# Optimization experiments

Hardware: AMD Instinct MI355X
Metric: run time of the kernel (lower is better)

## Reference

```python
import jax, jax.numpy as jnp
import numpy as np

# NF4 codebook (bitsandbytes nf4 data type, 16 levels)
NF4_TABLE = np.array([
    -1.0, -0.6961928009986877, -0.5250730514526367, -0.39491748809814453,
    -0.28444138169288635, -0.18477343022823334, -0.09105003625154495, 0.0,
    0.07958029955625534, 0.16093020141124725, 0.24611230194568634,
    0.33791524171829224, 0.44070982933044434, 0.5626170039176941,
    0.7229568362236023, 1.0], dtype=np.float32)

BLOCKSIZE = 64
SCALING = 32.0 / 16.0  # lora_alpha / r


def setup_inputs() -> dict:
    key = jax.random.key(0)
    k1, k2, k3, k4, k5 = jax.random.split(key, 5)
    tokens, in_f, out_f, r = 256, 4096, 11008, 16
    x = jax.random.normal(k1, (tokens, in_f), dtype=jnp.float32)
    q_codes = jax.random.randint(k2, (out_f, in_f), 0, 16, dtype=jnp.int32)
    absmax = jax.random.uniform(k3, (out_f, in_f // BLOCKSIZE), dtype=jnp.float32)
    lora_A = jax.random.normal(k4, (r, in_f), dtype=jnp.float32) * (1.0 / np.sqrt(in_f))
    lora_B = jax.random.normal(k5, (out_f, r), dtype=jnp.float32) * 0.02
    return {"x": x, "q_codes": q_codes, "absmax": absmax,
            "lora_A": lora_A, "lora_B": lora_B}


def reference(x, q_codes, absmax, lora_A, lora_B):
    out_f, in_f = q_codes.shape
    nf4 = jnp.asarray(NF4_TABLE, dtype=x.dtype)
    # Dequantize: codebook lookup, then per-block absmax scale.
    W = nf4[q_codes].reshape(out_f, in_f // BLOCKSIZE, BLOCKSIZE)
    W = (W * absmax[:, :, None]).reshape(out_f, in_f)  # [out_f, in_f]
    # Base 4-bit linear (no bias in bnb Linear4bit default here).
    base = x @ W.T  # [tokens, out_f]
    # LoRA path: dropout p=0 is identity in eval; scaling = alpha/r.
    lora = (x @ lora_A.T) @ lora_B.T  # [tokens, r] -> [tokens, out_f]
    return base + lora * jnp.asarray(SCALING, dtype=x.dtype)
```

## Files before the change

kernel.cpp:

```cpp
#include <hip/hip_runtime.h>
#include <hip/hip_fp16.h>

typedef unsigned int uint;
typedef unsigned short ushort;

typedef __attribute__((ext_vector_type(8))) _Float16 f16x8;
typedef __attribute__((ext_vector_type(4))) float f32x4;

#define TOK 256
#define OUTF 11008
#define INF 4096
#define BM 256
#define BN 64
#define NT2 172

__device__ __constant__ float NF4_TBL[16] = {
    -1.0f, -0.6961928009986877f, -0.5250730514526367f, -0.39491748809814453f,
    -0.28444138169288635f, -0.18477343022823334f, -0.09105003625154495f, 0.0f,
    0.07958029955625534f, 0.16093020141124725f, 0.24611230194568634f,
    0.33791524171829224f, 0.44070982933044434f, 0.5626170039176941f,
    0.7229568362236023f, 1.0f};

__device__ __forceinline__ ushort f2h(float f) {
  return __half_as_ushort(__float2half(f));
}

__device__ __forceinline__ void async_cp16(const void* g, void* l) {
  __builtin_amdgcn_global_load_lds(
      (const __attribute__((address_space(1))) uint*)g,
      (__attribute__((address_space(3))) uint*)l, 16, 0, 0);
}

__global__ void prep_kernel(const int4* __restrict__ qc4, uint* __restrict__ pk,
                            const float4* __restrict__ x4, ushort4* __restrict__ xh4,
                            const float4* __restrict__ lB4, ushort4* __restrict__ lBh4) {
  const int stride = gridDim.x * blockDim.x;
  const int t0 = blockIdx.x * blockDim.x + threadIdx.x;
  for (int d = t0; d < OUTF * INF / 8; d += stride) {
    int4 a = qc4[2 * d];
    int4 b = qc4[2 * d + 1];
    pk[d] = (uint)(a.x & 15) | ((uint)(a.y & 15) << 4) | ((uint)(a.z & 15) << 8) |
            ((uint)(a.w & 15) << 12) | ((uint)(b.x & 15) << 16) | ((uint)(b.y & 15) << 20) |
            ((uint)(b.z & 15) << 24) | ((uint)(b.w & 15) << 28);
  }
  for (int i = t0; i < TOK * INF / 4; i += stride) {
    float4 v = x4[i];
    ushort4 o;
    o.x = f2h(v.x); o.y = f2h(v.y); o.z = f2h(v.z); o.w = f2h(v.w);
    xh4[i] = o;
  }
  for (int i = t0; i < OUTF * 16; i += stride) {
    int n = i >> 4, jq = i & 15;
    ushort4 o = {0, 0, 0, 0};
    if (jq < 4) {
      float4 v = lB4[n * 4 + jq];
      o.x = f2h(v.x); o.y = f2h(v.y); o.z = f2h(v.z); o.w = f2h(v.w);
    }
    lBh4[i] = o;
  }
}

__global__ __launch_bounds__(1024)
void xa_kernel(const float* __restrict__ x, const float* __restrict__ lA,
               ushort* __restrict__ xa2) {
  const int m = blockIdx.x;
  const int t = threadIdx.x;
  const float4* x4 = (const float4*)(x + (size_t)m * INF);
  const float4* lA4 = (const float4*)lA;
  float4 xv = x4[t];
  float acc[16];
#pragma unroll
  for (int j = 0; j < 16; ++j) {
    float4 a = lA4[j * (INF / 4) + t];
    acc[j] = xv.x * a.x + xv.y * a.y + xv.z * a.z + xv.w * a.w;
  }
#pragma unroll
  for (int j = 0; j < 16; ++j)
#pragma unroll
    for (int s = 32; s > 0; s >>= 1) acc[j] += __shfl_xor(acc[j], s, 64);
  __shared__ float red[16][16];
  const int w = t >> 6, l = t & 63;
  if (l == 0) {
#pragma unroll
    for (int j = 0; j < 16; ++j) red[w][j] = acc[j];
  }
  __syncthreads();
  if (t < 64) {
    ushort v = 0;
    if (t < 16) {
      float s = 0.f;
#pragma unroll
      for (int w2 = 0; w2 < 16; ++w2) s += red[w2][t];
      v = f2h(2.0f * s);
    }
    xa2[m * 64 + t] = v;
  }
}

__global__ __launch_bounds__(256, 3)
void gemm_kernel(const uint* __restrict__ pk, const float* __restrict__ am,
                 const ushort* __restrict__ xh, const ushort* __restrict__ lBh,
                 const ushort* __restrict__ xa2, float* __restrict__ dest, int nst) {
  __shared__ ushort Abuf[BM * 64];
  __shared__ __half2 tbl[256];

  const int tid = threadIdx.x;
  const int w = tid >> 6;
  const int l = tid & 63;
  const int chunk = l >> 4;
  const int rlo = l & 15;
  const int split = blockIdx.x / NT2;
  const int ntile = blockIdx.x - split * NT2;
  const int n0 = ntile * BN;
  const int k0 = split * nst * 64;

  tbl[tid & 255] = __halves2half2(__float2half(NF4_TBL[tid & 15]),
                                  __float2half(NF4_TBL[(tid >> 4) & 15]));

  const int arow = w * 8 + (l >> 3);
  const int acol = ((l & 7) ^ (l >> 3)) << 3;

  int aoff[2][4];
#pragma unroll
  for (int ks = 0; ks < 2; ++ks) {
    const int cc = ks * 4 + chunk;
#pragma unroll
    for (int mt = 0; mt < 4; ++mt)
      aoff[ks][mt] = (w * 64 + mt * 16 + rlo) * 64 + ((cc ^ (l & 7)) << 3);
  }

  int col[4];
  const char* qp[4];
  const float* amp[4];
#pragma unroll
  for (int nt = 0; nt < 4; ++nt) {
    col[nt] = n0 + nt * 16 + rlo;
    qp[nt] = (const char*)pk + (size_t)col[nt] * (INF / 2) + (k0 >> 1) + chunk * 4;
    amp[nt] = am + (size_t)col[nt] * 64 + (k0 >> 6);
  }

  f32x4 acc[4][4];
#pragma unroll
  for (int mt = 0; mt < 4; ++mt)
#pragma unroll
    for (int nt = 0; nt < 4; ++nt) acc[mt][nt] = (f32x4){0.f, 0.f, 0.f, 0.f};

  for (int s = 0; s < nst; ++s) {
    const int kb = k0 + s * 64;
#pragma unroll
    for (int i = 0; i < 8; ++i) {
      const ushort* g = xh + (size_t)(i * 32 + arow) * INF + kb + acol;
      async_cp16(g, &Abuf[(i * 256 + w * 64) * 8]);
    }
    uint qd[4][2];
    __half2 ax2[4];
#pragma unroll
    for (int nt = 0; nt < 4; ++nt) {
      qd[nt][0] = *(const uint*)(qp[nt] + s * 32);
      qd[nt][1] = *(const uint*)(qp[nt] + s * 32 + 16);
      ax2[nt] = __float2half2_rn(amp[nt][s]);
    }
    __syncthreads();
#pragma unroll
    for (int ks = 0; ks < 2; ++ks) {
      f16x8 a[4];
#pragma unroll
      for (int mt = 0; mt < 4; ++mt) a[mt] = *(const f16x8*)&Abuf[aoff[ks][mt]];
      f16x8 b[4];
#pragma unroll
      for (int nt = 0; nt < 4; ++nt) {
        uint dw = qd[nt][ks];
        union { __half2 h[4]; f16x8 v; } u;
        u.h[0] = __hmul2(tbl[dw & 255], ax2[nt]);
        u.h[1] = __hmul2(tbl[(dw >> 8) & 255], ax2[nt]);
        u.h[2] = __hmul2(tbl[(dw >> 16) & 255], ax2[nt]);
        u.h[3] = __hmul2(tbl[dw >> 24], ax2[nt]);
        b[nt] = u.v;
      }
#pragma unroll
      for (int mt = 0; mt < 4; ++mt)
#pragma unroll
        for (int nt = 0; nt < 4; ++nt)
          acc[mt][nt] = __builtin_amdgcn_mfma_f32_16x16x32_f16(a[mt], b[nt], acc[mt][nt], 0, 0, 0);
    }
    __syncthreads();
  }

  if (split == 0) {
    f16x8 a_l[4], b_l[4];
#pragma unroll
    for (int mt = 0; mt < 4; ++mt)
      a_l[mt] = *(const f16x8*)(xa2 + (size_t)(w * 64 + mt * 16 + rlo) * 64 + chunk * 8);
#pragma unroll
    for (int nt = 0; nt < 4; ++nt)
      b_l[nt] = *(const f16x8*)(lBh + (size_t)col[nt] * 64 + chunk * 8);
#pragma unroll
    for (int mt = 0; mt < 4; ++mt)
#pragma unroll
      for (int nt = 0; nt < 4; ++nt)
        acc[mt][nt] = __builtin_amdgcn_mfma_f32_16x16x32_f16(a_l[mt], b_l[nt], acc[mt][nt], 0, 0, 0);
  }

  float* dst = dest + (size_t)split * TOK * OUTF;
#pragma unroll
  for (int mt = 0; mt < 4; ++mt) {
#pragma unroll
    for (int nt = 0; nt < 4; ++nt) {
      int c = col[nt];
#pragma unroll
      for (int r = 0; r < 4; ++r) {
        int row = w * 64 + mt * 16 + chunk * 4 + r;
        dst[(size_t)row * OUTF + c] = acc[mt][nt][r];
      }
    }
  }
}

__global__ void reduce_kernel(const float4* __restrict__ part, float4* __restrict__ out,
                              int ks) {
  const int QN = TOK * OUTF / 4;
  int i = blockIdx.x * blockDim.x + threadIdx.x;
  if (i < QN) {
    float4 s = part[i];
    for (int s2 = 1; s2 < ks; ++s2) {
      float4 p = part[(size_t)s2 * QN + i];
      s.x += p.x; s.y += p.y; s.z += p.z; s.w += p.w;
    }
    out[i] = s;
  }
}

extern "C" void kernel_launch(void* const* d_in, const int* in_sizes, int n_in,
                              void* d_out, int out_size, void* d_ws, size_t ws_size,
                              hipStream_t stream) {
  const float* x = (const float*)d_in[0];
  const int* qc = (const int*)d_in[1];
  const float* am = (const float*)d_in[2];
  const float* lA = (const float*)d_in[3];
  const float* lB = (const float*)d_in[4];
  float* out = (float*)d_out;

  const size_t off_lB = (size_t)TOK * INF * 2;
  const size_t off_xa2 = off_lB + (size_t)OUTF * 64 * 2;
  const size_t off_pk = off_xa2 + (size_t)TOK * 64 * 2;
  const size_t off_part = off_pk + (size_t)OUTF * INF / 2;
  const size_t part_bytes = (size_t)TOK * OUTF * 4;

  ushort* xh = (ushort*)d_ws;
  ushort* lBh = (ushort*)((char*)d_ws + off_lB);
  ushort* xa2 = (ushort*)((char*)d_ws + off_xa2);
  uint* pk = (uint*)((char*)d_ws + off_pk);
  float* part = (float*)((char*)d_ws + off_part);

  int ks = 1;
  if (ws_size >= off_part + 4 * part_bytes) ks = 4;
  else if (ws_size >= off_part + 2 * part_bytes) ks = 2;
  float* dest = (ks == 1) ? out : part;

  prep_kernel<<<4096, 256, 0, stream>>>((const int4*)qc, pk, (const float4*)x,
                                        (ushort4*)xh, (const float4*)lB, (ushort4*)lBh);
  xa_kernel<<<TOK, 1024, 0, stream>>>(x, lA, xa2);
  gemm_kernel<<<NT2 * ks, 256, 0, stream>>>(pk, am, xh, lBh, xa2, dest, 64 / ks);
  if (ks > 1)
    reduce_kernel<<<(TOK * OUTF / 4 + 255) / 256, 256, 0, stream>>>((const float4*)part,
                                                                    (float4*)out, ks);
}
```

Measured before the change: 371.2 us.

## Load activation tiles directly to registers with prefetch and drop LDS staging

The GEMM kernel no longer stages the fp16 activation tile in shared memory through async copies. Each wave now reads its own activation rows straight from global memory into registers, one 32-wide k-slice ahead. The packed NF4 codes and absmax scales are register double-buffered two steps ahead, which removes both per-iteration block barriers and hides load latency behind the MFMAs. The costs are higher register pressure (launch bounds lowered from 3 to 2 blocks per CU), less coalesced 16-byte global loads, and prefetch reads that run past each split's k-range into adjacent workspace memory.

```diff
diff --git a/kernel.cpp b/kernel.cpp
--- a/kernel.cpp
+++ b/kernel.cpp
@@ -10,7 +10,6 @@
 #define TOK 256
 #define OUTF 11008
 #define INF 4096
-#define BM 256
 #define BN 64
 #define NT2 172
 
@@ -23,12 +22,6 @@
 
 __device__ __forceinline__ ushort f2h(float f) {
   return __half_as_ushort(__float2half(f));
-}
-
-__device__ __forceinline__ void async_cp16(const void* g, void* l) {
-  __builtin_amdgcn_global_load_lds(
-      (const __attribute__((address_space(1))) uint*)g,
-      (__attribute__((address_space(3))) uint*)l, 16, 0, 0);
 }
 
 __global__ void prep_kernel(const int4* __restrict__ qc4, uint* __restrict__ pk,
@@ -97,11 +90,10 @@
   }
 }
 
-__global__ __launch_bounds__(256, 3)
+__global__ __launch_bounds__(256, 2)
 void gemm_kernel(const uint* __restrict__ pk, const float* __restrict__ am,
                  const ushort* __restrict__ xh, const ushort* __restrict__ lBh,
                  const ushort* __restrict__ xa2, float* __restrict__ dest, int nst) {
-  __shared__ ushort Abuf[BM * 64];
   __shared__ __half2 tbl[256];
 
   const int tid = threadIdx.x;
@@ -116,18 +108,12 @@
 
   tbl[tid & 255] = __halves2half2(__float2half(NF4_TBL[tid & 15]),
                                   __float2half(NF4_TBL[(tid >> 4) & 15]));
-
-  const int arow = w * 8 + (l >> 3);
-  const int acol = ((l & 7) ^ (l >> 3)) << 3;
-
-  int aoff[2][4];
-#pragma unroll
-  for (int ks = 0; ks < 2; ++ks) {
-    const int cc = ks * 4 + chunk;
-#pragma unroll
-    for (int mt = 0; mt < 4; ++mt)
-      aoff[ks][mt] = (w * 64 + mt * 16 + rlo) * 64 + ((cc ^ (l & 7)) << 3);
-  }
+  __syncthreads();
+
+  const ushort* aptr[4];
+#pragma unroll
+  for (int mt = 0; mt < 4; ++mt)
+    aptr[mt] = xh + (size_t)(w * 64 + mt * 16 + rlo) * INF + chunk * 8 + k0;
 
   int col[4];
   const char* qp[4];
@@ -145,45 +131,56 @@
 #pragma unroll
     for (int nt = 0; nt < 4; ++nt) acc[mt][nt] = (f32x4){0.f, 0.f, 0.f, 0.f};
 
+  uint qd[2][8];
+  float ax[2][4];
+#pragma unroll
+  for (int p = 0; p < 2; ++p)
+#pragma unroll
+    for (int nt = 0; nt < 4; ++nt) {
+      qd[p][nt * 2 + 0] = *(const uint*)(qp[nt] + p * 32);
+      qd[p][nt * 2 + 1] = *(const uint*)(qp[nt] + p * 32 + 16);
+      ax[p][nt] = amp[nt][p];
+    }
+  f16x8 aC[4];
+#pragma unroll
+  for (int mt = 0; mt < 4; ++mt) aC[mt] = *(const f16x8*)(aptr[mt]);
+
+#pragma unroll 2
   for (int s = 0; s < nst; ++s) {
-    const int kb = k0 + s * 64;
-#pragma unroll
-    for (int i = 0; i < 8; ++i) {
-      const ushort* g = xh + (size_t)(i * 32 + arow) * INF + kb + acol;
-      async_cp16(g, &Abuf[(i * 256 + w * 64) * 8]);
-    }
-    uint qd[4][2];
-    __half2 ax2[4];
-#pragma unroll
-    for (int nt = 0; nt < 4; ++nt) {
-      qd[nt][0] = *(const uint*)(qp[nt] + s * 32);
-      qd[nt][1] = *(const uint*)(qp[nt] + s * 32 + 16);
-      ax2[nt] = __float2half2_rn(amp[nt][s]);
-    }
-    __syncthreads();
-#pragma unroll
-    for (int ks = 0; ks < 2; ++ks) {
-      f16x8 a[4];
-#pragma unroll
-      for (int mt = 0; mt < 4; ++mt) a[mt] = *(const f16x8*)&Abuf[aoff[ks][mt]];
+    const int par = s & 1;
+#pragma unroll
+    for (int sub = 0; sub < 2; ++sub) {
+      const int kn = (s * 2 + sub + 1) * 32;
+      f16x8 aN[4];
+#pragma unroll
+      for (int mt = 0; mt < 4; ++mt) aN[mt] = *(const f16x8*)(aptr[mt] + kn);
       f16x8 b[4];
 #pragma unroll
       for (int nt = 0; nt < 4; ++nt) {
-        uint dw = qd[nt][ks];
+        uint dw = qd[par][nt * 2 + sub];
+        __half2 ax2 = __float2half2_rn(ax[par][nt]);
         union { __half2 h[4]; f16x8 v; } u;
-        u.h[0] = __hmul2(tbl[dw & 255], ax2[nt]);
-        u.h[1] = __hmul2(tbl[(dw >> 8) & 255], ax2[nt]);
-        u.h[2] = __hmul2(tbl[(dw >> 16) & 255], ax2[nt]);
-        u.h[3] = __hmul2(tbl[dw >> 24], ax2[nt]);
+        u.h[0] = __hmul2(tbl[dw & 255], ax2);
+        u.h[1] = __hmul2(tbl[(dw >> 8) & 255], ax2);
+        u.h[2] = __hmul2(tbl[(dw >> 16) & 255], ax2);
+        u.h[3] = __hmul2(tbl[dw >> 24], ax2);
         b[nt] = u.v;
       }
 #pragma unroll
       for (int mt = 0; mt < 4; ++mt)
 #pragma unroll
         for (int nt = 0; nt < 4; ++nt)
-          acc[mt][nt] = __builtin_amdgcn_mfma_f32_16x16x32_f16(a[mt], b[nt], acc[mt][nt], 0, 0, 0);
-    }
-    __syncthreads();
+          acc[mt][nt] = __builtin_amdgcn_mfma_f32_16x16x32_f16(aC[mt], b[nt], acc[mt][nt], 0, 0, 0);
+#pragma unroll
+      for (int mt = 0; mt < 4; ++mt) aC[mt] = aN[mt];
+    }
+    const int am_i = (s + 2 < nst) ? (s + 2) : 0;
+#pragma unroll
+    for (int nt = 0; nt < 4; ++nt) {
+      qd[par][nt * 2 + 0] = *(const uint*)(qp[nt] + (s + 2) * 32);
+      qd[par][nt * 2 + 1] = *(const uint*)(qp[nt] + (s + 2) * 32 + 16);
+      ax[par][nt] = amp[nt][am_i];
+    }
   }
 
   if (split == 0) {
```

Result: slower. 435.2 us (+17.2%).

## Prefetch next K-stage A tile and quant codes while computing current stage

Applied to the files above, without the earlier changes.

Restructures the GEMM main loop so that the A tile is copied from LDS into registers, after which the async global-to-LDS copy for the next stage is issued and the next stage's packed codes and absmax are prefetched into double-buffered registers. The MFMA work then runs on register-held data, overlapping global latency with compute. It also allows an 8-way K split when the workspace is large enough, giving more blocks but more partial-sum traffic in the reduce step. The cost is higher register pressure from holding both A subtiles and two sets of codes.

```diff
diff --git a/kernel.cpp b/kernel.cpp
--- a/kernel.cpp
+++ b/kernel.cpp
@@ -122,11 +122,11 @@
 
   int aoff[2][4];
 #pragma unroll
-  for (int ks = 0; ks < 2; ++ks) {
-    const int cc = ks * 4 + chunk;
+  for (int ks2 = 0; ks2 < 2; ++ks2) {
+    const int cc = ks2 * 4 + chunk;
 #pragma unroll
     for (int mt = 0; mt < 4; ++mt)
-      aoff[ks][mt] = (w * 64 + mt * 16 + rlo) * 64 + ((cc ^ (l & 7)) << 3);
+      aoff[ks2][mt] = (w * 64 + mt * 16 + rlo) * 64 + ((cc ^ (l & 7)) << 3);
   }
 
   int col[4];
@@ -145,45 +145,69 @@
 #pragma unroll
     for (int nt = 0; nt < 4; ++nt) acc[mt][nt] = (f32x4){0.f, 0.f, 0.f, 0.f};
 
+#pragma unroll
+  for (int i = 0; i < 8; ++i) {
+    const ushort* g = xh + (size_t)(i * 32 + arow) * INF + k0 + acol;
+    async_cp16(g, &Abuf[(i * 256 + w * 64) * 8]);
+  }
+  uint qd[2][8];
+  float ax[2][4];
+#pragma unroll
+  for (int nt = 0; nt < 4; ++nt) {
+    qd[0][nt * 2 + 0] = *(const uint*)(qp[nt]);
+    qd[0][nt * 2 + 1] = *(const uint*)(qp[nt] + 16);
+    ax[0][nt] = amp[nt][0];
+  }
+
+#pragma unroll 2
   for (int s = 0; s < nst; ++s) {
-    const int kb = k0 + s * 64;
-#pragma unroll
-    for (int i = 0; i < 8; ++i) {
-      const ushort* g = xh + (size_t)(i * 32 + arow) * INF + kb + acol;
-      async_cp16(g, &Abuf[(i * 256 + w * 64) * 8]);
-    }
-    uint qd[4][2];
-    __half2 ax2[4];
+    const int p = s & 1;
+    __syncthreads();
+
+    f16x8 areg[2][4];
+#pragma unroll
+    for (int ks2 = 0; ks2 < 2; ++ks2)
+#pragma unroll
+      for (int mt = 0; mt < 4; ++mt) areg[ks2][mt] = *(const f16x8*)&Abuf[aoff[ks2][mt]];
+
+    __syncthreads();
+
+    if (s + 1 < nst) {
+      const int kb = k0 + (s + 1) * 64;
+#pragma unroll
+      for (int i = 0; i < 8; ++i) {
+        const ushort* g = xh + (size_t)(i * 32 + arow) * INF + kb + acol;
+        async_cp16(g, &Abuf[(i * 256 + w * 64) * 8]);
+      }
+    }
+    const int sq = (s + 1 < nst) ? (s + 1) : (nst - 1);
 #pragma unroll
     for (int nt = 0; nt < 4; ++nt) {
-      qd[nt][0] = *(const uint*)(qp[nt] + s * 32);
-      qd[nt][1] = *(const uint*)(qp[nt] + s * 32 + 16);
-      ax2[nt] = __float2half2_rn(amp[nt][s]);
-    }
-    __syncthreads();
-#pragma unroll
-    for (int ks = 0; ks < 2; ++ks) {
-      f16x8 a[4];
-#pragma unroll
-      for (int mt = 0; mt < 4; ++mt) a[mt] = *(const f16x8*)&Abuf[aoff[ks][mt]];
+      qd[p ^ 1][nt * 2 + 0] = *(const uint*)(qp[nt] + sq * 32);
+      qd[p ^ 1][nt * 2 + 1] = *(const uint*)(qp[nt] + sq * 32 + 16);
+      ax[p ^ 1][nt] = amp[nt][sq];
+    }
+
+#pragma unroll
+    for (int ks2 = 0; ks2 < 2; ++ks2) {
       f16x8 b[4];
 #pragma unroll
       for (int nt = 0; nt < 4; ++nt) {
-        uint dw = qd[nt][ks];
+        uint dw = qd[p][nt * 2 + ks2];
+        __half2 ax2 = __float2half2_rn(ax[p][nt]);
         union { __half2 h[4]; f16x8 v; } u;
-        u.h[0] = __hmul2(tbl[dw & 255], ax2[nt]);
-        u.h[1] = __hmul2(tbl[(dw >> 8) & 255], ax2[nt]);
-        u.h[2] = __hmul2(tbl[(dw >> 16) & 255], ax2[nt]);
-        u.h[3] = __hmul2(tbl[dw >> 24], ax2[nt]);
+        u.h[0] = __hmul2(tbl[dw & 255], ax2);
+        u.h[1] = __hmul2(tbl[(dw >> 8) & 255], ax2);
+        u.h[2] = __hmul2(tbl[(dw >> 16) & 255], ax2);
+        u.h[3] = __hmul2(tbl[dw >> 24], ax2);
         b[nt] = u.v;
       }
 #pragma unroll
       for (int mt = 0; mt < 4; ++mt)
 #pragma unroll
         for (int nt = 0; nt < 4; ++nt)
-          acc[mt][nt] = __builtin_amdgcn_mfma_f32_16x16x32_f16(a[mt], b[nt], acc[mt][nt], 0, 0, 0);
-    }
-    __syncthreads();
+          acc[mt][nt] = __builtin_amdgcn_mfma_f32_16x16x32_f16(areg[ks2][mt], b[nt], acc[mt][nt], 0, 0, 0);
+    }
   }
 
   if (split == 0) {
@@ -253,7 +277,8 @@
   float* part = (float*)((char*)d_ws + off_part);
 
   int ks = 1;
-  if (ws_size >= off_part + 4 * part_bytes) ks = 4;
+  if (ws_size >= off_part + 8 * part_bytes) ks = 8;
+  else if (ws_size >= off_part + 4 * part_bytes) ks = 4;
   else if (ws_size >= off_part + 2 * part_bytes) ks = 2;
   float* dest = (ks == 1) ? out : part;
 
```

New measurement: 386.5 us. 4.1% more time.
